# Performance work log

Measured on AMD Instinct MI355X. Metric: run time of the kernel, lower is better.

The kernel has to match this reference:

```python
import jax, jax.numpy as jnp
import numpy as np

BATCH, SEQ, IN_F, OUT_F, RES, N_EXP, TOP_K = 4, 2048, 4096, 4096, 64, 16, 2


def setup_inputs() -> dict:
    key = jax.random.key(0)
    k0, k1, k2, k3, k4 = jax.random.split(key, 5)
    x = jax.random.normal(k0, (BATCH, SEQ, IN_F), dtype=jnp.float32)
    W_base = jax.random.normal(k1, (OUT_F, IN_F), dtype=jnp.float32) * 0.02
    b_base = jnp.zeros((OUT_F,), dtype=jnp.float32)
    # get_orthogonal_matrix(reservoir_size, in_features): rows orthonormal
    A = jnp.linalg.qr(jax.random.normal(k2, (IN_F, RES), dtype=jnp.float32))[0].T  # [RES, IN_F]
    # B is zero-init in the module; use small random so delta is non-trivial for testing
    B = jax.random.normal(k3, (N_EXP, OUT_F, RES), dtype=jnp.float32) * 0.01
    W_router = jax.random.normal(k4, (N_EXP, IN_F), dtype=jnp.float32) * 0.02
    return {"x": x, "W_base": W_base, "b_base": b_base, "A": A, "B": B,
            "W_router": W_router, "top_k": TOP_K}


def reference(x, W_base, b_base, A, B, W_router, top_k):
    n_experts = W_router.shape[0]
    base_out = jnp.einsum('bsi,oi->bso', x, W_base) + b_base          # [B,S,OUT]
    res_hidden = jnp.einsum('bsi,ri->bsr', x, A)                      # [B,S,RES]
    router_logits = jnp.einsum('bsi,ni->bsn', x, W_router)            # [B,S,N]
    routing = jax.nn.softmax(router_logits, axis=-1)
    if 0 < top_k < n_experts:
        _, top_idx = jax.lax.top_k(routing, top_k)                    # [B,S,K]
        mask = jax.nn.one_hot(top_idx, n_experts, dtype=routing.dtype).sum(axis=-2)
        routing = routing * mask
        routing = routing / (routing.sum(axis=-1, keepdims=True) + 1e-6)
    delta = jnp.einsum('bsr,bsn,ndr->bsd', res_hidden, routing, B)    # [B,S,OUT]
    return base_out + delta
```

## Files before the change

### kernel.cpp

```cpp
#include <hip/hip_runtime.h>
#include <hip/hip_bf16.h>
#include <cstdint>
#include <cmath>


#define M_TOT 8192
#define N_OUT 4096
#define K_IN  4096
#define K_TOT 5120
#define NEXP  16
#define NRES  64
#define NT    (K_TOT / 64)
#define NCH   (K_IN / 64)

typedef __bf16 bf16x8 __attribute__((ext_vector_type(8)));
typedef float  f32x4  __attribute__((ext_vector_type(4)));
using u16 = unsigned short;

__device__ __forceinline__ u16 bfbits(float f) {
  __bf16 h = (__bf16)f;
  union { __bf16 h; u16 u; } c; c.h = h;
  return c.u;
}
__device__ __forceinline__ float lopart(float f) {
  __bf16 h = (__bf16)f;
  return f - (float)h;
}

__device__ __forceinline__ void gload_lds16(const void* g, void* l) {
  const __attribute__((address_space(1))) unsigned* gp =
      (const __attribute__((address_space(1))) unsigned*)(unsigned long long)(uintptr_t)g;
  __attribute__((address_space(3))) unsigned* lp =
      (__attribute__((address_space(3))) unsigned*)(unsigned)(uintptr_t)l;
  __builtin_amdgcn_global_load_lds(gp, lp, 16, 0, 0);
}

#define MFMA16 __builtin_amdgcn_mfma_f32_16x16x32_bf16

__global__ __launch_bounds__(256) void build_msp(const float* __restrict__ Wr,
                                                 const float* __restrict__ Amat,
                                                 u16* __restrict__ Msp) {
  const int row = blockIdx.x;
  const int tid = threadIdx.x;
  const float* src = (row < 16) ? (Wr + (size_t)row * K_IN)
                   : (row < 80) ? (Amat + (size_t)(row - 16) * K_IN)
                                : (Wr + (size_t)(row - 80) * K_IN);
  const bool lo = (row >= 80);
#pragma unroll
  for (int it = 0; it < 2; ++it) {
    int gi = tid + it * 256;
    int col = gi * 8;
    float4 a = *(const float4*)(src + col);
    float4 b = *(const float4*)(src + col + 4);
    float v0 = a.x, v1 = a.y, v2 = a.z, v3 = a.w;
    float v4 = b.x, v5 = b.y, v6 = b.z, v7 = b.w;
    if (lo) { v0 = lopart(v0); v1 = lopart(v1); v2 = lopart(v2); v3 = lopart(v3);
              v4 = lopart(v4); v5 = lopart(v5); v6 = lopart(v6); v7 = lopart(v7); }
    ushort4 o0, o1;
    o0.x = bfbits(v0); o0.y = bfbits(v1); o0.z = bfbits(v2); o0.w = bfbits(v3);
    o1.x = bfbits(v4); o1.y = bfbits(v5); o1.z = bfbits(v6); o1.w = bfbits(v7);
    u16* dst = Msp + ((size_t)(((gi >> 3) * 96 + row) * 8 + ((gi & 7) ^ (row & 7)))) * 8;
    *(ushort4*)(dst) = o0;
    *(ushort4*)(dst + 4) = o1;
  }
}

#define PSTR 72
#define BUF_U16 10752

__global__ __launch_bounds__(256) void prep_fused(const float* __restrict__ x,
                                                  const u16* __restrict__ Msp,
                                                  const int* __restrict__ topk_p,
                                                  const float* __restrict__ Wb,
                                                  const float* __restrict__ Bm,
                                                  u16* __restrict__ Xa,
                                                  u16* __restrict__ Wa) {
  __shared__ __align__(16) u16 smem[2 * BUF_U16];
  const int tid = threadIdx.x;

  if (blockIdx.x >= 256) {
    const int d = blockIdx.x - 256;
#pragma unroll
    for (int it = 0; it < 5; ++it) {
      int j = tid + it * 256;
      int kcol = j * 4;
      float4 v;
      if (kcol < K_IN) {
        v = *(const float4*)(Wb + (size_t)d * K_IN + kcol);
      } else {
        int kk = kcol - K_IN;
        int n = kk >> 6, r = kk & 63;
        v = *(const float4*)(Bm + ((size_t)n * N_OUT + d) * NRES + r);
      }
      ushort4 o;
      o.x = bfbits(v.x); o.y = bfbits(v.y); o.z = bfbits(v.z); o.w = bfbits(v.w);
      *(ushort4*)(Wa + (size_t)d * K_TOT + kcol) = o;
    }
    return;
  }

  const int w = tid >> 6, l = tid & 63;
  const int l15 = l & 15, l4 = l >> 4;
  const int rt = w >> 1, cg = w & 1;
  const int token0 = blockIdx.x * 32;

  f32x4 acc[3] = {};

#define STAGE_CHUNK(kc, buf) do {                                              \
    u16* xh_ = smem + (buf) * BUF_U16;                                         \
    u16* xl_ = xh_ + 32 * PSTR;                                                \
    u16* Ms_ = xl_ + 32 * PSTR;                                                \
    const int k0_ = (kc) * 64;                                                 \
    _Pragma("unroll")                                                          \
    for (int it = 0; it < 3; ++it) {                                           \
      gload_lds16(Msp + (size_t)(kc) * 6144 + (size_t)(it * 256 + tid) * 8,    \
                  Ms_ + it * 2048 + w * 512);                                  \
    }                                                                          \
    _Pragma("unroll")                                                          \
    for (int it = 0; it < 2; ++it) {                                           \
      int i_ = tid + it * 256;                                                 \
      int row_ = i_ >> 4, c4_ = (i_ & 15) * 4;                                 \
      float4 v_ = *(const float4*)(x + (size_t)(token0 + row_) * K_IN + k0_ + c4_); \
      ushort4 h_;                                                              \
      h_.x = bfbits(v_.x); h_.y = bfbits(v_.y);                                \
      h_.z = bfbits(v_.z); h_.w = bfbits(v_.w);                                \
      ushort4 lo_;                                                             \
      lo_.x = bfbits(lopart(v_.x)); lo_.y = bfbits(lopart(v_.y));              \
      lo_.z = bfbits(lopart(v_.z)); lo_.w = bfbits(lopart(v_.w));              \
      *(ushort4*)&xh_[row_ * PSTR + c4_] = h_;                                 \
      *(ushort4*)&xl_[row_ * PSTR + c4_] = lo_;                                \
      *(ushort4*)(Xa + (size_t)(token0 + row_) * K_TOT + k0_ + c4_) = h_;      \
    }                                                                          \
  } while (0)

#define MS_FRAG(Ms_, tb, ks) \
  (*(const bf16x8*)&(Ms_)[(size_t)((((tb) * 16 + l15) * 8 + (((ks) * 4 + l4) ^ (l15 & 7)))) * 8])

  STAGE_CHUNK(0, 0);
  __syncthreads();

  for (int kc = 0; kc < NCH; ++kc) {
    const int cur = kc & 1;
    if (kc + 1 < NCH) {
      if ((kc + 1) & 1) STAGE_CHUNK(kc + 1, 1);
      else              STAGE_CHUNK(kc + 1, 0);
    }
    {
      const u16* xh_ = smem + cur * BUF_U16;
      const u16* xl_ = xh_ + 32 * PSTR;
      const u16* Ms_ = xl_ + 32 * PSTR;
      const int arow = (rt * 16 + l15) * PSTR;
#pragma unroll
      for (int ks = 0; ks < 2; ++ks) {
        const int fo = ks * 32 + l4 * 8;
        const bf16x8 ah = *(const bf16x8*)&xh_[arow + fo];
        if (cg == 0) {
          const bf16x8 al = *(const bf16x8*)&xl_[arow + fo];
          const bf16x8 b0 = MS_FRAG(Ms_, 0, ks);
          const bf16x8 b1 = MS_FRAG(Ms_, 1, ks);
          const bf16x8 b5 = MS_FRAG(Ms_, 5, ks);
          acc[0] = MFMA16(ah, b0, acc[0], 0, 0, 0);
          acc[0] = MFMA16(al, b0, acc[0], 0, 0, 0);
          acc[0] = MFMA16(ah, b5, acc[0], 0, 0, 0);
          acc[1] = MFMA16(ah, b1, acc[1], 0, 0, 0);
        } else {
          const bf16x8 b2 = MS_FRAG(Ms_, 2, ks);
          const bf16x8 b3 = MS_FRAG(Ms_, 3, ks);
          const bf16x8 b4 = MS_FRAG(Ms_, 4, ks);
          acc[0] = MFMA16(ah, b2, acc[0], 0, 0, 0);
          acc[1] = MFMA16(ah, b3, acc[1], 0, 0, 0);
          acc[2] = MFMA16(ah, b4, acc[2], 0, 0, 0);
        }
      }
    }
    __syncthreads();
  }

  float* arr  = (float*)smem;
  float* wexp = (float*)((char*)smem + 10240);
  {
    const int row0 = rt * 16 + l4 * 4;
    if (cg == 0) {
#pragma unroll
      for (int ct = 0; ct < 2; ++ct)
#pragma unroll
        for (int j = 0; j < 4; ++j)
          arr[(row0 + j) * 80 + ct * 16 + l15] = acc[ct][j];
    } else {
#pragma unroll
      for (int ct = 0; ct < 3; ++ct)
#pragma unroll
        for (int j = 0; j < 4; ++j)
          arr[(row0 + j) * 80 + 32 + ct * 16 + l15] = acc[ct][j];
    }
  }
  __syncthreads();

  if (tid < 32) {
    const int tt = tid;
    const int k = *topk_p;
    float p[16];
    float mx = arr[tt * 80 + 0];
#pragma unroll
    for (int e = 1; e < 16; ++e) mx = fmaxf(mx, arr[tt * 80 + e]);
    float Z = 0.f;
#pragma unroll
    for (int e = 0; e < 16; ++e) { p[e] = expf(arr[tt * 80 + e] - mx); Z += p[e]; }
    const float invZ = 1.f / Z;
#pragma unroll
    for (int e = 0; e < 16; ++e) p[e] *= invZ;
    float wv[16];
    if (k <= 0 || k >= NEXP) {
#pragma unroll
      for (int e = 0; e < 16; ++e) wv[e] = p[e];
    } else {
      unsigned um = 0; float ssum = 0.f;
      for (int kk = 0; kk < k; ++kk) {
        int best = 0; float bv = -1.f;
#pragma unroll
        for (int e = 0; e < 16; ++e)
          if (!((um >> e) & 1u) && p[e] > bv) { bv = p[e]; best = e; }
        um |= 1u << best; ssum += bv;
      }
      const float inv = 1.f / (ssum + 1e-6f);
#pragma unroll
      for (int e = 0; e < 16; ++e) wv[e] = ((um >> e) & 1u) ? p[e] * inv : 0.f;
    }
#pragma unroll
    for (int e = 0; e < 16; ++e) wexp[tt * 16 + e] = wv[e];
  }
  __syncthreads();

#pragma unroll
  for (int it = 0; it < 16; ++it) {
    int idx = tid + it * 256;
    int tt = idx >> 7, c8 = idx & 127;
    int n = c8 >> 3, r0 = (c8 & 7) * 8;
    const float wv = wexp[tt * 16 + n];
    const float* hb = &arr[tt * 80 + 16 + r0];
    ushort4 lo, hi;
    lo.x = bfbits(wv * hb[0]); lo.y = bfbits(wv * hb[1]);
    lo.z = bfbits(wv * hb[2]); lo.w = bfbits(wv * hb[3]);
    hi.x = bfbits(wv * hb[4]); hi.y = bfbits(wv * hb[5]);
    hi.z = bfbits(wv * hb[6]); hi.w = bfbits(wv * hb[7]);
    u16* dst = Xa + (size_t)(token0 + tt) * K_TOT + K_IN + c8 * 8;
    *(ushort4*)(dst) = lo;
    *(ushort4*)(dst + 4) = hi;
  }
}

#define PHASE_BAR() do {                      \
  __builtin_amdgcn_sched_barrier(0);          \
  __builtin_amdgcn_s_barrier();               \
  __builtin_amdgcn_sched_barrier(0);          \
} while (0)

#define LGKM0() do {                          \
  asm volatile("s_waitcnt lgkmcnt(0)");       \
  __builtin_amdgcn_sched_barrier(0);          \
} while (0)

__global__ __launch_bounds__(512, 2) void gemm_aug(const u16* __restrict__ Xa,
                                                   const u16* __restrict__ Wa,
                                                   const float* __restrict__ bias,
                                                   float* __restrict__ out) {
  extern __shared__ u16 lds[];
  const int tid = threadIdx.x;
  const int w = tid >> 6, l = tid & 63;
  const int bid = blockIdx.x;
  const int wg = (bid & 7) * 64 + (bid >> 3);
  const int bm = wg >> 4, bn = wg & 15;
  const int wm = w >> 2, wn = w & 3;

  const int srow = w * 8 + (l >> 3);
  const int gsw = ((l & 7) ^ (l >> 3)) * 8;
  const u16* sA = Xa + (size_t)(bm * 256 + srow) * K_TOT + gsw;
  const u16* sB = Wa + (size_t)(bn * 256 + srow) * K_TOT + gsw;
  const int stq = w * 512;

  const int arow = (l & 15) * 64;
  const int c0 = (((l >> 4) + 0) ^ (l & 7)) * 8;
  const int c1 = (((l >> 4) + 4) ^ (l & 7)) * 8;

  f32x4 acc[8][4] = {};

#define STAGE_A2(tile, half, bufc) do {                                        \
    const u16* s_ = sA + (size_t)(half) * 128 * K_TOT + (size_t)(tile) * 64;   \
    const int d_ = (bufc) * 32768 + (half) * 8192 + stq;                       \
    gload_lds16(s_, &lds[d_]);                                                 \
    gload_lds16(s_ + (size_t)64 * K_TOT, &lds[d_ + 4096]);                     \
  } while (0)
#define STAGE_B2(tile, half, bufc) do {                                        \
    const u16* s_ = sB + (size_t)(half) * 128 * K_TOT + (size_t)(tile) * 64;   \
    const int d_ = (bufc) * 32768 + 16384 + (half) * 8192 + stq;               \
    gload_lds16(s_, &lds[d_]);                                                 \
    gload_lds16(s_ + (size_t)64 * K_TOT, &lds[d_ + 4096]);                     \
  } while (0)

  STAGE_B2(0, 0, 0); STAGE_B2(0, 1, 0); STAGE_A2(0, 0, 0); STAGE_A2(0, 1, 0);
  STAGE_B2(1, 0, 1); STAGE_B2(1, 1, 1); STAGE_A2(1, 0, 1);
  __builtin_amdgcn_sched_barrier(0);
  asm volatile("s_waitcnt vmcnt(6)");
  PHASE_BAR();

#define DO_TILE(TT, BUFC) do {                                                 \
    const int aoff_ = (BUFC) * 32768 + wm * 8192;                              \
    const int boff_ = (BUFC) * 32768 + 16384 + (wn >> 1) * 8192 + (wn & 1) * 4096; \
    bf16x8 af[4][2], b0f[2][2], b1f[2][2];                                     \
     \
    _Pragma("unroll")                                                          \
    for (int m = 0; m < 4; ++m) {                                              \
      af[m][0] = *(const bf16x8*)&lds[aoff_ + m * 1024 + arow + c0];           \
      af[m][1] = *(const bf16x8*)&lds[aoff_ + m * 1024 + arow + c1];           \
    }                                                                          \
    _Pragma("unroll")                                                          \
    for (int n = 0; n < 2; ++n) {                                              \
      b0f[n][0] = *(const bf16x8*)&lds[boff_ + n * 1024 + arow + c0];          \
      b0f[n][1] = *(const bf16x8*)&lds[boff_ + n * 1024 + arow + c1];          \
    }                                                                          \
    if ((TT) + 1 < NT) STAGE_A2((TT) + 1, 1, (BUFC) ^ 1);                      \
    PHASE_BAR(); LGKM0();                                                      \
    __builtin_amdgcn_s_setprio(1);                                             \
    _Pragma("unroll")                                                          \
    for (int m = 0; m < 4; ++m)                                                \
      _Pragma("unroll")                                                        \
      for (int n = 0; n < 2; ++n) {                                            \
        acc[m][n] = MFMA16(af[m][0], b0f[n][0], acc[m][n], 0, 0, 0);           \
        acc[m][n] = MFMA16(af[m][1], b0f[n][1], acc[m][n], 0, 0, 0);           \
      }                                                                        \
    __builtin_amdgcn_s_setprio(0);                                             \
                             \
    _Pragma("unroll")                                                          \
    for (int n = 0; n < 2; ++n) {                                              \
      b1f[n][0] = *(const bf16x8*)&lds[boff_ + (n + 2) * 1024 + arow + c0];    \
      b1f[n][1] = *(const bf16x8*)&lds[boff_ + (n + 2) * 1024 + arow + c1];    \
    }                                                                          \
    PHASE_BAR(); LGKM0();                                                      \
    __builtin_amdgcn_s_setprio(1);                                             \
    _Pragma("unroll")                                                          \
    for (int m = 0; m < 4; ++m)                                                \
      _Pragma("unroll")                                                        \
      for (int n = 0; n < 2; ++n) {                                            \
        acc[m][n + 2] = MFMA16(af[m][0], b1f[n][0], acc[m][n + 2], 0, 0, 0);   \
        acc[m][n + 2] = MFMA16(af[m][1], b1f[n][1], acc[m][n + 2], 0, 0, 0);   \
      }                                                                        \
    __builtin_amdgcn_s_setprio(0);                                             \
                     \
    _Pragma("unroll")                                                          \
    for (int m = 0; m < 4; ++m) {                                              \
      af[m][0] = *(const bf16x8*)&lds[aoff_ + 4096 + m * 1024 + arow + c0];    \
      af[m][1] = *(const bf16x8*)&lds[aoff_ + 4096 + m * 1024 + arow + c1];    \
    }                                                                          \
    if ((TT) + 2 < NT) STAGE_B2((TT) + 2, 0, (BUFC));                          \
    PHASE_BAR(); LGKM0();                                                      \
    __builtin_amdgcn_s_setprio(1);                                             \
    _Pragma("unroll")                                                          \
    for (int m = 0; m < 4; ++m)                                                \
      _Pragma("unroll")                                                        \
      for (int n = 0; n < 2; ++n) {                                            \
        acc[m + 4][n + 2] = MFMA16(af[m][0], b1f[n][0], acc[m + 4][n + 2], 0, 0, 0); \
        acc[m + 4][n + 2] = MFMA16(af[m][1], b1f[n][1], acc[m + 4][n + 2], 0, 0, 0); \
      }                                                                        \
    __builtin_amdgcn_s_setprio(0);                                             \
           \
    if ((TT) + 2 < NT) {                                                       \
      STAGE_B2((TT) + 2, 1, (BUFC));                                           \
      STAGE_A2((TT) + 2, 0, (BUFC));                                           \
      __builtin_amdgcn_sched_barrier(0);                                       \
      asm volatile("s_waitcnt vmcnt(6)");                                      \
    } else {                                                                   \
      asm volatile("s_waitcnt vmcnt(0)");                                      \
    }                                                                          \
    PHASE_BAR();                                                               \
    __builtin_amdgcn_s_setprio(1);                                             \
    _Pragma("unroll")                                                          \
    for (int m = 0; m < 4; ++m)                                                \
      _Pragma("unroll")                                                        \
      for (int n = 0; n < 2; ++n) {                                            \
        acc[m + 4][n] = MFMA16(af[m][0], b0f[n][0], acc[m + 4][n], 0, 0, 0);   \
        acc[m + 4][n] = MFMA16(af[m][1], b0f[n][1], acc[m + 4][n], 0, 0, 0);   \
      }                                                                        \
    __builtin_amdgcn_s_setprio(0);                                             \
  } while (0)

  for (int t = 0; t < NT; t += 2) {
    DO_TILE(t, 0);
    DO_TILE(t + 1, 1);
  }

  const int colBase = bn * 256 + wn * 64 + (l & 15);
  float bv[4];
#pragma unroll
  for (int n = 0; n < 4; ++n) bv[n] = bias[colBase + n * 16];
#pragma unroll
  for (int mi = 0; mi < 8; ++mi) {
    const int row = bm * 256 + wm * 128 + mi * 16 + (l >> 4) * 4;
#pragma unroll
    for (int j = 0; j < 4; ++j) {
      float* orow = out + (size_t)(row + j) * N_OUT + colBase;
#pragma unroll
      for (int n = 0; n < 4; ++n) orow[n * 16] = acc[mi][n][j] + bv[n];
    }
  }
}

extern "C" void kernel_launch(void* const* d_in, const int* in_sizes, int n_in,
                              void* d_out, int out_size, void* d_ws, size_t ws_size,
                              hipStream_t stream) {
  const float* x  = (const float*)d_in[0];
  const float* Wb = (const float*)d_in[1];
  const float* bb = (const float*)d_in[2];
  const float* Am = (const float*)d_in[3];
  const float* Bm = (const float*)d_in[4];
  const float* Wr = (const float*)d_in[5];
  const int* topk = (const int*)d_in[6];
  float* out = (float*)d_out;

  u16* Xa  = (u16*)d_ws;
  u16* Wa  = Xa + (size_t)M_TOT * K_TOT;
  u16* Msp = Wa + (size_t)N_OUT * K_TOT;

  (void)hipFuncSetAttribute((const void*)gemm_aug,
                            hipFuncAttributeMaxDynamicSharedMemorySize, 131072);

  hipLaunchKernelGGL(build_msp,  dim3(96),         dim3(256), 0, stream,
                     Wr, Am, Msp);
  hipLaunchKernelGGL(prep_fused, dim3(256 + N_OUT), dim3(256), 0, stream,
                     x, Msp, topk, Wb, Bm, Xa, Wa);
  hipLaunchKernelGGL(gemm_aug,   dim3(512),        dim3(512), 131072, stream,
                     Xa, Wa, bb, out);
}
```

Measured before the change: 359.6 us.

## Simplify GEMM main loop to plain double buffering with two phases

Replaces the four-phase interleaved pipeline, which prefetched two tiles ahead and staggered the staging across phases, with a simple double-buffer scheme. Each tile issues all loads for the next tile up front, reads the full A fragment set (8 rows) and all B fragments into registers, then runs two MFMA phases with a full vmcnt(0) wait between them. This reduces the number of barriers and phases, but loses the deeper prefetch distance. It also raises register pressure because the A fragments are doubled, which risks exposing memory latency.

```diff
diff --git a/kernel.cpp b/kernel.cpp
--- a/kernel.cpp
+++ b/kernel.cpp
@@ -298,18 +298,23 @@
   } while (0)
 
   STAGE_B2(0, 0, 0); STAGE_B2(0, 1, 0); STAGE_A2(0, 0, 0); STAGE_A2(0, 1, 0);
-  STAGE_B2(1, 0, 1); STAGE_B2(1, 1, 1); STAGE_A2(1, 0, 1);
   __builtin_amdgcn_sched_barrier(0);
-  asm volatile("s_waitcnt vmcnt(6)");
+  asm volatile("s_waitcnt vmcnt(0)");
   PHASE_BAR();
 
 #define DO_TILE(TT, BUFC) do {                                                 \
     const int aoff_ = (BUFC) * 32768 + wm * 8192;                              \
     const int boff_ = (BUFC) * 32768 + 16384 + (wn >> 1) * 8192 + (wn & 1) * 4096; \
-    bf16x8 af[4][2], b0f[2][2], b1f[2][2];                                     \
-     \
-    _Pragma("unroll")                                                          \
-    for (int m = 0; m < 4; ++m) {                                              \
+    bf16x8 af[8][2], b0f[2][2], b1f[2][2];                                     \
+              \
+    if ((TT) + 1 < NT) {                                                       \
+      STAGE_B2((TT) + 1, 0, (BUFC) ^ 1);                                       \
+      STAGE_B2((TT) + 1, 1, (BUFC) ^ 1);                                       \
+      STAGE_A2((TT) + 1, 0, (BUFC) ^ 1);                                       \
+      STAGE_A2((TT) + 1, 1, (BUFC) ^ 1);                                       \
+    }                                                                          \
+    _Pragma("unroll")                                                          \
+    for (int m = 0; m < 8; ++m) {                                              \
       af[m][0] = *(const bf16x8*)&lds[aoff_ + m * 1024 + arow + c0];           \
       af[m][1] = *(const bf16x8*)&lds[aoff_ + m * 1024 + arow + c1];           \
     }                                                                          \
@@ -317,68 +322,30 @@
     for (int n = 0; n < 2; ++n) {                                              \
       b0f[n][0] = *(const bf16x8*)&lds[boff_ + n * 1024 + arow + c0];          \
       b0f[n][1] = *(const bf16x8*)&lds[boff_ + n * 1024 + arow + c1];          \
-    }                                                                          \
-    if ((TT) + 1 < NT) STAGE_A2((TT) + 1, 1, (BUFC) ^ 1);                      \
+      b1f[n][0] = *(const bf16x8*)&lds[boff_ + (n + 2) * 1024 + arow + c0];    \
+      b1f[n][1] = *(const bf16x8*)&lds[boff_ + (n + 2) * 1024 + arow + c1];    \
+    }                                                                          \
     PHASE_BAR(); LGKM0();                                                      \
     __builtin_amdgcn_s_setprio(1);                                             \
     _Pragma("unroll")                                                          \
-    for (int m = 0; m < 4; ++m)                                                \
+    for (int m = 0; m < 8; ++m)                                                \
       _Pragma("unroll")                                                        \
       for (int n = 0; n < 2; ++n) {                                            \
         acc[m][n] = MFMA16(af[m][0], b0f[n][0], acc[m][n], 0, 0, 0);           \
         acc[m][n] = MFMA16(af[m][1], b0f[n][1], acc[m][n], 0, 0, 0);           \
       }                                                                        \
     __builtin_amdgcn_s_setprio(0);                                             \
-                             \
-    _Pragma("unroll")                                                          \
-    for (int n = 0; n < 2; ++n) {                                              \
-      b1f[n][0] = *(const bf16x8*)&lds[boff_ + (n + 2) * 1024 + arow + c0];    \
-      b1f[n][1] = *(const bf16x8*)&lds[boff_ + (n + 2) * 1024 + arow + c1];    \
-    }                                                                          \
-    PHASE_BAR(); LGKM0();                                                      \
+      \
+    __builtin_amdgcn_sched_barrier(0);                                         \
+    asm volatile("s_waitcnt vmcnt(0)");                                        \
+    PHASE_BAR();                                                               \
     __builtin_amdgcn_s_setprio(1);                                             \
     _Pragma("unroll")                                                          \
-    for (int m = 0; m < 4; ++m)                                                \
+    for (int m = 0; m < 8; ++m)                                                \
       _Pragma("unroll")                                                        \
       for (int n = 0; n < 2; ++n) {                                            \
         acc[m][n + 2] = MFMA16(af[m][0], b1f[n][0], acc[m][n + 2], 0, 0, 0);   \
         acc[m][n + 2] = MFMA16(af[m][1], b1f[n][1], acc[m][n + 2], 0, 0, 0);   \
-      }                                                                        \
-    __builtin_amdgcn_s_setprio(0);                                             \
-                     \
-    _Pragma("unroll")                                                          \
-    for (int m = 0; m < 4; ++m) {                                              \
-      af[m][0] = *(const bf16x8*)&lds[aoff_ + 4096 + m * 1024 + arow + c0];    \
-      af[m][1] = *(const bf16x8*)&lds[aoff_ + 4096 + m * 1024 + arow + c1];    \
-    }                                                                          \
-    if ((TT) + 2 < NT) STAGE_B2((TT) + 2, 0, (BUFC));                          \
-    PHASE_BAR(); LGKM0();                                                      \
-    __builtin_amdgcn_s_setprio(1);                                             \
-    _Pragma("unroll")                                                          \
-    for (int m = 0; m < 4; ++m)                                                \
-      _Pragma("unroll")                                                        \
-      for (int n = 0; n < 2; ++n) {                                            \
-        acc[m + 4][n + 2] = MFMA16(af[m][0], b1f[n][0], acc[m + 4][n + 2], 0, 0, 0); \
-        acc[m + 4][n + 2] = MFMA16(af[m][1], b1f[n][1], acc[m + 4][n + 2], 0, 0, 0); \
-      }                                                                        \
-    __builtin_amdgcn_s_setprio(0);                                             \
-           \
-    if ((TT) + 2 < NT) {                                                       \
-      STAGE_B2((TT) + 2, 1, (BUFC));                                           \
-      STAGE_A2((TT) + 2, 0, (BUFC));                                           \
-      __builtin_amdgcn_sched_barrier(0);                                       \
-      asm volatile("s_waitcnt vmcnt(6)");                                      \
-    } else {                                                                   \
-      asm volatile("s_waitcnt vmcnt(0)");                                      \
-    }                                                                          \
-    PHASE_BAR();                                                               \
-    __builtin_amdgcn_s_setprio(1);                                             \
-    _Pragma("unroll")                                                          \
-    for (int m = 0; m < 4; ++m)                                                \
-      _Pragma("unroll")                                                        \
-      for (int n = 0; n < 2; ++n) {                                            \
-        acc[m + 4][n] = MFMA16(af[m][0], b0f[n][0], acc[m + 4][n], 0, 0, 0);   \
-        acc[m + 4][n] = MFMA16(af[m][1], b0f[n][1], acc[m + 4][n], 0, 0, 0);   \
       }                                                                        \
     __builtin_amdgcn_s_setprio(0);                                             \
   } while (0)
@@ -423,10 +390,10 @@
   (void)hipFuncSetAttribute((const void*)gemm_aug,
                             hipFuncAttributeMaxDynamicSharedMemorySize, 131072);
 
-  hipLaunchKernelGGL(build_msp,  dim3(96),         dim3(256), 0, stream,
+  hipLaunchKernelGGL(build_msp,  dim3(96),          dim3(256), 0, stream,
                      Wr, Am, Msp);
   hipLaunchKernelGGL(prep_fused, dim3(256 + N_OUT), dim3(256), 0, stream,
                      x, Msp, topk, Wb, Bm, Xa, Wa);
-  hipLaunchKernelGGL(gemm_aug,   dim3(512),        dim3(512), 131072, stream,
+  hipLaunchKernelGGL(gemm_aug,   dim3(512),         dim3(512), 131072, stream,
                      Xa, Wa, bb, out);
 }
```

Measured after the change: 417.0 us. 16.0% more time.
